# Performance work log

Hardware: AMD Instinct MI355X
Metric: run time of the kernel (lower is better)

## Reference

```python
import jax, jax.numpy as jnp
import numpy as np


def setup_inputs() -> dict:
    key = jax.random.key(0)
    ks = jax.random.split(key, 5)
    B, T, I, H = 64, 2048, 512, 512
    s_in = 1.0 / np.sqrt(I)
    s_h = 1.0 / np.sqrt(H)
    return {
        "x": jax.random.normal(ks[0], (B, T, I), dtype=jnp.float32),
        "Wx": jax.random.normal(ks[1], (4 * H, I), dtype=jnp.float32) * s_in,
        "bx": jax.random.normal(ks[2], (4 * H,), dtype=jnp.float32) * s_in,
        "Wh": jax.random.normal(ks[3], (4 * H, H), dtype=jnp.float32) * s_h,
        "bh": jax.random.normal(ks[4], (4 * H,), dtype=jnp.float32) * s_h,
    }


def reference(x, Wx, bx, Wh, bh):
    B, T, I = x.shape
    H = Wh.shape[1]
    # Precompute input projections for all timesteps (same math, batched GEMM).
    # gates_x: (T, B, 4H)
    gates_x = jnp.einsum('bti,gi->tbg', x, Wx) + bx + bh

    def step(carry, gx):
        h, c = carry
        gates = gx + h @ Wh.T  # (B, 4H)
        i, f, g, o = jnp.split(gates, 4, axis=1)
        i = jax.nn.sigmoid(i)
        f = jax.nn.sigmoid(f)
        g = jnp.tanh(g)
        o = jax.nn.sigmoid(o)
        c = f * c + i * g
        h = o * jnp.tanh(c)
        return (h, c), h

    h0 = jnp.zeros((B, H), dtype=x.dtype)
    c0 = jnp.zeros((B, H), dtype=x.dtype)
    (h_n, c_n), out = jax.lax.scan(step, (h0, c0), gates_x)
    output = jnp.transpose(out, (1, 0, 2))  # (B, T, H)
    return output, (h_n, c_n)
```

## Files before the change

kernel.cpp:

```cpp
#include <hip/hip_runtime.h>
#include <stdint.h>

typedef unsigned short u16;
typedef unsigned int   u32;
typedef unsigned long long u64;

#define B_  64
#define T_  2048
#define I_  512
#define H_  512
#define G_  2048

typedef __attribute__((ext_vector_type(8))) __bf16 bf16x8;
typedef __attribute__((ext_vector_type(4))) float  f32x4;

#define OFF_XB    0ull
#define OFF_GX    134217728ull
#define OFF_WXP   (OFF_GX + 536870912ull)
#define OFF_WHP   (OFF_WXP + 2097152ull)
#define OFF_BIAS  (OFF_WHP + 2097152ull)
#define OFF_HBUF  (OFF_BIAS + 8192ull)
#define WS_NEEDED (OFF_HBUF + 262144ull)

__device__ __forceinline__ float bf2f(u16 u) {
  union { float f; u32 u; } c; c.u = ((u32)u) << 16; return c.f;
}
__device__ __forceinline__ u16 f2bf(float f) {
  union { float f; u32 u; } c; c.f = f;
  u32 u = c.u;
  return (u16)((u + 0x7FFFu + ((u >> 16) & 1u)) >> 16);
}
__device__ __forceinline__ float sigmoidf_(float x) {
  return __fdividef(1.f, 1.f + __expf(-x));
}
__device__ __forceinline__ float tanhf_(float x) {
  return 1.f - __fdividef(2.f, 1.f + __expf(2.f * x));
}
__device__ __forceinline__ void async16(const u16* g, u16* l) {
  __builtin_amdgcn_global_load_lds((const __attribute__((address_space(1))) void*)g,
                                   (__attribute__((address_space(3))) void*)l,
                                   16, 0, 0);
}

__global__ void __launch_bounds__(256)
prep_misc(const float* __restrict__ wx, const float* __restrict__ bx,
          const float* __restrict__ wh, const float* __restrict__ bh,
          u16* __restrict__ wxp, u16* __restrict__ whp,
          float* __restrict__ bias, u32* __restrict__ hbuf0)
{
  int idx = blockIdx.x * 256 + threadIdx.x;
  int n = idx >> 9, k = idx & 511;
  long r = (long)(((n & 3) << 9) | (n >> 2)) * 512 + k;
  wxp[idx] = f2bf(wx[r]);
  whp[idx] = f2bf(wh[r]);
  if (idx < G_) {
    int rb = ((idx & 3) << 9) | (idx >> 2);
    bias[idx] = bx[rb] + bh[rb];
  }
  if (idx < 65536) hbuf0[idx] = 0u;
}

__global__ void __launch_bounds__(256)
conv_x(const float* __restrict__ x, u16* __restrict__ xb)
{
  long idx = ((long)blockIdx.x * 256 + threadIdx.x) * 4;
  float4 v = *(const float4*)(x + idx);
  u64 pk = (u64)f2bf(v.x) | ((u64)f2bf(v.y) << 16) |
           ((u64)f2bf(v.z) << 32) | ((u64)f2bf(v.w) << 48);
  *(u64*)(xb + idx) = pk;
}

__global__ void __launch_bounds__(256)
gemm_gates(const u16* __restrict__ xb, const u16* __restrict__ wxp,
           const float* __restrict__ bias, u16* __restrict__ gx)
{
  __shared__ __align__(16) u16 smem[16384];
  const int tid  = threadIdx.x;
  const int lane = tid & 63;
  const int w    = tid >> 6;
  const int tn   = blockIdx.x;
  const int tm   = blockIdx.y;
  const int wr   = w >> 1, wc = w & 1;

  const u16* gsrc[8];
  u16* ldst[8];
#pragma unroll
  for (int q = 0; q < 8; ++q) {
    int c   = w * 8 + q;
    int isB = c >= 16;
    int cc  = c & 15;
    int rloc = (cc >> 1) * 16 + (lane & 15);
    int koff = (cc & 1) * 32 + ((lane >> 4) << 3);
    if (!isB) {
      int m = tm * 128 + rloc;
      int bb = m & 63, tt = m >> 6;
      gsrc[q] = xb + (long)bb * (T_ * I_) + (long)tt * I_ + koff;
    } else {
      int n = tn * 128 + rloc;
      gsrc[q] = wxp + (long)n * I_ + koff;
    }
    ldst[q] = smem + isB * 8192 + cc * 512;
  }

  f32x4 acc[4][4] = {};
  for (int k0 = 0; k0 < I_; k0 += 64) {
#pragma unroll
    for (int q = 0; q < 8; ++q) async16(gsrc[q] + k0, ldst[q]);
    __syncthreads();
#pragma unroll
    for (int kb = 0; kb < 2; ++kb) {
      bf16x8 a[4], b[4];
#pragma unroll
      for (int i = 0; i < 4; ++i)
        a[i] = *(const bf16x8*)(smem + ((wr * 4 + i) * 2 + kb) * 512 + lane * 8);
#pragma unroll
      for (int j = 0; j < 4; ++j)
        b[j] = *(const bf16x8*)(smem + 8192 + ((wc * 4 + j) * 2 + kb) * 512 + lane * 8);
#pragma unroll
      for (int i = 0; i < 4; ++i)
#pragma unroll
        for (int j = 0; j < 4; ++j)
          acc[i][j] = __builtin_amdgcn_mfma_f32_16x16x32_bf16(a[i], b[j], acc[i][j], 0, 0, 0);
    }
    __syncthreads();
  }

#pragma unroll
  for (int j = 0; j < 4; ++j) {
    int n = tn * 128 + (wc * 4 + j) * 16 + (lane & 15);
    float bv = bias[n];
#pragma unroll
    for (int i = 0; i < 4; ++i) {
      int mbase = tm * 128 + (wr * 4 + i) * 16 + ((lane >> 4) << 2);
#pragma unroll
      for (int r = 0; r < 4; ++r) {
        int m = mbase + r;
        int tt = m >> 6, bb = m & 63;
        gx[(long)tt * (B_ * G_) + (long)bb * G_ + n] = f2bf(acc[i][j][r] + bv);
      }
    }
  }
}

__global__ void __launch_bounds__(256)
lstm_rec(const u16* __restrict__ gx, const u16* __restrict__ whp,
         u64* hbuf, float* __restrict__ out)
{
  __shared__ __align__(16) char lds[32768 + 8192];
  u16*  Hs  = (u16*)lds;
  float* scr = (float*)(lds + 32768);

  const int tid  = threadIdx.x;
  const int lane = tid & 63;
  const int w    = tid >> 6;
  const int bg   = blockIdx.x >> 4;
  const int kg   = blockIdx.x & 15;

  bf16x8 wf0[16], wf1[16];
  {
    const int n0   = kg * 128 + (2 * w) * 16 + (lane & 15);
    const int koff = (lane >> 4) << 3;
#pragma unroll
    for (int kb = 0; kb < 16; ++kb) {
      wf0[kb] = *(const bf16x8*)(whp + (long)n0 * 512 + kb * 32 + koff);
      wf1[kb] = *(const bf16x8*)(whp + (long)(n0 + 16) * 512 + kb * 32 + koff);
    }
  }

  const int srow = tid >> 4;
  const u64* hsrc = hbuf + (long)(bg * 16 + srow) * 256 + (tid & 15);
  const int sl = srow + (((tid & 15) >> 2) << 4);
  u16* sdst = Hs + sl * 8 + 2 * (tid & 3);

  const int id    = lane * 2;
  const int b16   = id >> 3;
  const int klw   = id & 7;
  const int kl    = w * 8 + klw;
  const int kgl   = kg * 32 + kl;
  const int bglob = bg * 16 + b16;

  const u16* gxp0 = gx + (long)bglob * G_ + (long)kgl * 4;
  uint4 gq = *(const uint4*)gxp0;

  u64* hdst = hbuf + (long)bglob * 256 + (kgl >> 1);
  float c0 = 0.f, c1 = 0.f;

  for (int t = 0; t < T_; ++t) {
    const int par = t & 1;

    const u64* hp_ = hsrc + (size_t)par * 16384;
    u64 v[16];
    for (;;) {
      bool ok = true;
#pragma unroll
      for (int s = 0; s < 16; ++s)
        v[s] = __hip_atomic_load(hp_ + s * 16, __ATOMIC_RELAXED, __HIP_MEMORY_SCOPE_AGENT);
#pragma unroll
      for (int s = 0; s < 16; ++s) ok &= ((u32)v[s] == (u32)t);
      if (ok) break;
      __builtin_amdgcn_s_sleep(1);
    }

    u16* sd = sdst + par * 8192;
#pragma unroll
    for (int s = 0; s < 16; ++s)
      *(u32*)(sd + s * 512) = (u32)(v[s] >> 32);
    __syncthreads();

    const u16* Hb = Hs + par * 8192;
    f32x4 acc0a = {0.f,0.f,0.f,0.f}, acc0b = {0.f,0.f,0.f,0.f};
    f32x4 acc1a = {0.f,0.f,0.f,0.f}, acc1b = {0.f,0.f,0.f,0.f};
#pragma unroll
    for (int kb = 0; kb < 16; kb += 2) {
      bf16x8 aA = *(const bf16x8*)(Hb + kb * 512 + lane * 8);
      bf16x8 aB = *(const bf16x8*)(Hb + (kb + 1) * 512 + lane * 8);
      acc0a = __builtin_amdgcn_mfma_f32_16x16x32_bf16(aA, wf0[kb],     acc0a, 0, 0, 0);
      acc1a = __builtin_amdgcn_mfma_f32_16x16x32_bf16(aA, wf1[kb],     acc1a, 0, 0, 0);
      acc0b = __builtin_amdgcn_mfma_f32_16x16x32_bf16(aB, wf0[kb + 1], acc0b, 0, 0, 0);
      acc1b = __builtin_amdgcn_mfma_f32_16x16x32_bf16(aB, wf1[kb + 1], acc1b, 0, 0, 0);
    }
    f32x4 acc0 = acc0a + acc0b;
    f32x4 acc1 = acc1a + acc1b;

    float* sw = scr + w * 512;
    {
      const int colq = (lane & 15) >> 2;
      const int gidx = lane & 3;
      const int bq   = (lane >> 4) << 2;
#pragma unroll
      for (int r = 0; r < 4; ++r) {
        sw[((bq + r) * 8 + colq) * 4 + gidx]     = acc0[r];
        sw[((bq + r) * 8 + 4 + colq) * 4 + gidx] = acc1[r];
      }
    }

    uint4 gqc = gq;
    if (t + 1 < T_) gq = *(const uint4*)(gxp0 + (long)(t + 1) * (B_ * G_));

    const u16* gu = (const u16*)&gqc;
    f32x4 ga = *(const f32x4*)(sw + (b16 * 8 + klw) * 4);
    f32x4 gb = *(const f32x4*)(sw + (b16 * 8 + klw + 1) * 4);

    float i0 = sigmoidf_(ga[0] + bf2f(gu[0]));
    float f0 = sigmoidf_(ga[1] + bf2f(gu[1]));
    float g0 = tanhf_   (ga[2] + bf2f(gu[2]));
    float o0 = sigmoidf_(ga[3] + bf2f(gu[3]));
    float i1 = sigmoidf_(gb[0] + bf2f(gu[4]));
    float f1 = sigmoidf_(gb[1] + bf2f(gu[5]));
    float g1 = tanhf_   (gb[2] + bf2f(gu[6]));
    float o1 = sigmoidf_(gb[3] + bf2f(gu[7]));
    float cn0 = f0 * c0 + i0 * g0;
    float cn1 = f1 * c1 + i1 * g1;
    float h0 = o0 * tanhf_(cn0);
    float h1 = o1 * tanhf_(cn1);
    c0 = cn0;
    c1 = cn1;

    u32 hp = ((u32)f2bf(h1) << 16) | (u32)f2bf(h0);
    u64 tv = ((u64)hp << 32) | (u32)(t + 1);
    __hip_atomic_store(hdst + (size_t)((t + 1) & 1) * 16384, tv,
                       __ATOMIC_RELAXED, __HIP_MEMORY_SCOPE_AGENT);

    float2 hv; hv.x = h0; hv.y = h1;
    *(float2*)(out + ((long)bglob * T_ + t) * H_ + kgl) = hv;

    if (t == T_ - 1) {
      float2 cv; cv.x = cn0; cv.y = cn1;
      *(float2*)(out + (size_t)B_ * T_ * H_ + (long)bglob * H_ + kgl) = hv;
      *(float2*)(out + (size_t)B_ * T_ * H_ + B_ * H_ + (long)bglob * H_ + kgl) = cv;
    }
  }
}

extern "C" void kernel_launch(void* const* d_in, const int* in_sizes, int n_in,
                              void* d_out, int out_size, void* d_ws, size_t ws_size,
                              hipStream_t stream)
{
  (void)in_sizes; (void)n_in; (void)out_size;
  if (ws_size < WS_NEEDED) return;

  const float* x  = (const float*)d_in[0];
  const float* Wx = (const float*)d_in[1];
  const float* bx = (const float*)d_in[2];
  const float* Wh = (const float*)d_in[3];
  const float* bh = (const float*)d_in[4];
  float* out = (float*)d_out;
  char* ws = (char*)d_ws;
  u16* xb     = (u16*)(ws + OFF_XB);
  u16* gx     = (u16*)(ws + OFF_GX);
  u16* wxp    = (u16*)(ws + OFF_WXP);
  u16* whp    = (u16*)(ws + OFF_WHP);
  float* bias = (float*)(ws + OFF_BIAS);
  u64* hbuf   = (u64*)(ws + OFF_HBUF);

  prep_misc<<<4096, 256, 0, stream>>>(Wx, bx, Wh, bh, wxp, whp, bias, (u32*)hbuf);
  conv_x<<<65536, 256, 0, stream>>>(x, xb);
  gemm_gates<<<dim3(16, 1024), 256, 0, stream>>>(xb, wxp, bias, gx);
  lstm_rec<<<64, 256, 0, stream>>>(gx, whp, hbuf, out);
}
```

Before: 5.729 ms.

## Skip own-slice global polling and prefetch next-step hidden-state flags early

```diff
diff --git a/kernel.cpp b/kernel.cpp
--- a/kernel.cpp
+++ b/kernel.cpp
@@ -142,11 +142,11 @@
   }
 }
 
-__global__ void __launch_bounds__(256)
+__global__ void __launch_bounds__(256, 1)
 lstm_rec(const u16* __restrict__ gx, const u16* __restrict__ whp,
          u64* hbuf, float* __restrict__ out)
 {
-  __shared__ __align__(16) char lds[32768 + 8192];
+  __shared__ __align__(16) char lds[32768 + 10240];
   u16*  Hs  = (u16*)lds;
   float* scr = (float*)(lds + 32768);
 
@@ -168,9 +168,10 @@
   }
 
   const int srow = tid >> 4;
-  const u64* hsrc = hbuf + (long)(bg * 16 + srow) * 256 + (tid & 15);
-  const int sl = srow + (((tid & 15) >> 2) << 4);
-  u16* sdst = Hs + sl * 8 + 2 * (tid & 3);
+  const int scol = tid & 15;
+  const u64* hsrc = hbuf + (long)(bg * 16 + srow) * 256 + scol;
+  const int sl = srow + ((scol >> 2) << 4);
+  u16* sdst = Hs + sl * 8 + 2 * (scol & 3);
 
   const int id    = lane * 2;
   const int b16   = id >> 3;
@@ -183,29 +184,46 @@
   uint4 gq = *(const uint4*)gxp0;
 
   u64* hdst = hbuf + (long)bglob * 256 + (kgl >> 1);
+  u16* ownw = Hs + kg * 512 + (b16 + (w << 4)) * 8 + klw;
   float c0 = 0.f, c1 = 0.f;
+
+  *(u32*)ownw = 0u;
+  u64 v[16];
+  v[0] = 0;
+#pragma unroll
+  for (int s = 0; s < 16; ++s)
+    if (s != kg)
+      v[s] = __hip_atomic_load(hsrc + s * 16, __ATOMIC_RELAXED, __HIP_MEMORY_SCOPE_AGENT);
 
   for (int t = 0; t < T_; ++t) {
     const int par = t & 1;
-
     const u64* hp_ = hsrc + (size_t)par * 16384;
-    u64 v[16];
-    for (;;) {
-      bool ok = true;
+
+    bool ok = true;
+#pragma unroll
+    for (int s = 0; s < 16; ++s)
+      if (s != kg) ok &= ((u32)v[s] == (u32)t);
+    while (!ok) {
+      __builtin_amdgcn_s_sleep(1);
 #pragma unroll
       for (int s = 0; s < 16; ++s)
-        v[s] = __hip_atomic_load(hp_ + s * 16, __ATOMIC_RELAXED, __HIP_MEMORY_SCOPE_AGENT);
-#pragma unroll
-      for (int s = 0; s < 16; ++s) ok &= ((u32)v[s] == (u32)t);
-      if (ok) break;
-      __builtin_amdgcn_s_sleep(1);
+        if (s != kg)
+          v[s] = __hip_atomic_load(hp_ + s * 16, __ATOMIC_RELAXED, __HIP_MEMORY_SCOPE_AGENT);
+      ok = true;
+#pragma unroll
+      for (int s = 0; s < 16; ++s)
+        if (s != kg) ok &= ((u32)v[s] == (u32)t);
     }
 
     u16* sd = sdst + par * 8192;
 #pragma unroll
     for (int s = 0; s < 16; ++s)
-      *(u32*)(sd + s * 512) = (u32)(v[s] >> 32);
+      if (s != kg)
+        *(u32*)(sd + s * 512) = (u32)(v[s] >> 32);
     __syncthreads();
+
+    uint4 gcur = gq;
+    if (t + 1 < T_) gq = *(const uint4*)(gxp0 + (long)(t + 1) * (B_ * G_));
 
     const u16* Hb = Hs + par * 8192;
     f32x4 acc0a = {0.f,0.f,0.f,0.f}, acc0b = {0.f,0.f,0.f,0.f};
@@ -222,24 +240,21 @@
     f32x4 acc0 = acc0a + acc0b;
     f32x4 acc1 = acc1a + acc1b;
 
-    float* sw = scr + w * 512;
+    float* sw = scr + w * 640;
     {
       const int colq = (lane & 15) >> 2;
       const int gidx = lane & 3;
       const int bq   = (lane >> 4) << 2;
 #pragma unroll
       for (int r = 0; r < 4; ++r) {
-        sw[((bq + r) * 8 + colq) * 4 + gidx]     = acc0[r];
-        sw[((bq + r) * 8 + 4 + colq) * 4 + gidx] = acc1[r];
+        sw[(bq + r) * 36 + colq * 4 + gidx]       = acc0[r];
+        sw[(bq + r) * 36 + (colq + 4) * 4 + gidx] = acc1[r];
       }
     }
 
-    uint4 gqc = gq;
-    if (t + 1 < T_) gq = *(const uint4*)(gxp0 + (long)(t + 1) * (B_ * G_));
-
-    const u16* gu = (const u16*)&gqc;
-    f32x4 ga = *(const f32x4*)(sw + (b16 * 8 + klw) * 4);
-    f32x4 gb = *(const f32x4*)(sw + (b16 * 8 + klw + 1) * 4);
+    const u16* gu = (const u16*)&gcur;
+    f32x4 ga = *(const f32x4*)(sw + b16 * 36 + klw * 4);
+    f32x4 gb = *(const f32x4*)(sw + b16 * 36 + (klw + 1) * 4);
 
     float i0 = sigmoidf_(ga[0] + bf2f(gu[0]));
     float f0 = sigmoidf_(ga[1] + bf2f(gu[1]));
@@ -256,10 +271,19 @@
     c0 = cn0;
     c1 = cn1;
 
+    if (t + 1 < T_) {
+      const u64* hn_ = hsrc + (size_t)((t + 1) & 1) * 16384;
+#pragma unroll
+      for (int s = 0; s < 16; ++s)
+        if (s != kg)
+          v[s] = __hip_atomic_load(hn_ + s * 16, __ATOMIC_RELAXED, __HIP_MEMORY_SCOPE_AGENT);
+    }
+
     u32 hp = ((u32)f2bf(h1) << 16) | (u32)f2bf(h0);
     u64 tv = ((u64)hp << 32) | (u32)(t + 1);
     __hip_atomic_store(hdst + (size_t)((t + 1) & 1) * 16384, tv,
                        __ATOMIC_RELAXED, __HIP_MEMORY_SCOPE_AGENT);
+    *(u32*)(ownw + ((t + 1) & 1) * 8192) = hp;
 
     float2 hv; hv.x = h0; hv.y = h1;
     *(float2*)(out + ((long)bglob * T_ + t) * H_ + kgl) = hv;
```

Result: slower. 7.863 ms (+37.3%).

## Stage recurrent weights in swizzled LDS and skip polling own h slice

Applied to the files above, without the earlier changes.

```diff
diff --git a/kernel.cpp b/kernel.cpp
--- a/kernel.cpp
+++ b/kernel.cpp
@@ -146,9 +146,10 @@
 lstm_rec(const u16* __restrict__ gx, const u16* __restrict__ whp,
          u64* hbuf, float* __restrict__ out)
 {
-  __shared__ __align__(16) char lds[32768 + 8192];
+  __shared__ __align__(16) char lds[16384 + 131072 + 10240];
   u16*  Hs  = (u16*)lds;
-  float* scr = (float*)(lds + 32768);
+  u16*  LWh = (u16*)(lds + 16384);
+  float* scr = (float*)(lds + 16384 + 131072);
 
   const int tid  = threadIdx.x;
   const int lane = tid & 63;
@@ -156,21 +157,28 @@
   const int bg   = blockIdx.x >> 4;
   const int kg   = blockIdx.x & 15;
 
-  bf16x8 wf0[16], wf1[16];
-  {
-    const int n0   = kg * 128 + (2 * w) * 16 + (lane & 15);
-    const int koff = (lane >> 4) << 3;
-#pragma unroll
-    for (int kb = 0; kb < 16; ++kb) {
-      wf0[kb] = *(const bf16x8*)(whp + (long)n0 * 512 + kb * 32 + koff);
-      wf1[kb] = *(const bf16x8*)(whp + (long)(n0 + 16) * 512 + kb * 32 + koff);
-    }
-  }
+  for (int c = tid; c < 8192; c += 256) {
+    int col = c >> 6;
+    int off = (c & 63) << 4;
+    bf16x8 vw = *(const bf16x8*)(whp + ((long)(kg * 128 + col) << 9) + (off >> 1));
+    *(bf16x8*)((char*)LWh + ((long)col << 10) + (off ^ ((col & 7) << 4))) = vw;
+  }
+
+  const int bcol0 = (w << 5) + (lane & 15);
+  const int bkoff = (lane >> 4) << 4;
+  const int wswz  = (bcol0 & 7) << 4;
+  const int bsw   = bkoff ^ (wswz & 0x30);
+  const char* wbase = (const char*)LWh + (bcol0 << 10);
+  const char* wb0e = wbase + bsw + (wswz & 0x40);
+  const char* wb0o = wbase + bsw - (wswz & 0x40);
+  const char* wb1e = wb0e + (16 << 10);
+  const char* wb1o = wb0o + (16 << 10);
 
   const int srow = tid >> 4;
-  const u64* hsrc = hbuf + (long)(bg * 16 + srow) * 256 + (tid & 15);
-  const int sl = srow + (((tid & 15) >> 2) << 4);
-  u16* sdst = Hs + sl * 8 + 2 * (tid & 3);
+  const int scol = tid & 15;
+  const u64* hsrc = hbuf + (long)(bg * 16 + srow) * 256 + scol;
+  const int sl = srow + ((scol >> 2) << 4);
+  u16* sdst = Hs + sl * 8 + 2 * (scol & 3);
 
   const int id    = lane * 2;
   const int b16   = id >> 3;
@@ -183,54 +191,64 @@
   uint4 gq = *(const uint4*)gxp0;
 
   u64* hdst = hbuf + (long)bglob * 256 + (kgl >> 1);
+  u16* ownw = Hs + kg * 512 + (b16 + (w << 4)) * 8 + klw;
   float c0 = 0.f, c1 = 0.f;
+
+  *(u32*)ownw = 0u;
 
   for (int t = 0; t < T_; ++t) {
     const int par = t & 1;
-
     const u64* hp_ = hsrc + (size_t)par * 16384;
+
     u64 v[16];
+    v[kg] = 0;
     for (;;) {
       bool ok = true;
 #pragma unroll
       for (int s = 0; s < 16; ++s)
-        v[s] = __hip_atomic_load(hp_ + s * 16, __ATOMIC_RELAXED, __HIP_MEMORY_SCOPE_AGENT);
-#pragma unroll
-      for (int s = 0; s < 16; ++s) ok &= ((u32)v[s] == (u32)t);
+        if (s != kg)
+          v[s] = __hip_atomic_load(hp_ + s * 16, __ATOMIC_RELAXED, __HIP_MEMORY_SCOPE_AGENT);
+#pragma unroll
+      for (int s = 0; s < 16; ++s)
+        if (s != kg) ok &= ((u32)v[s] == (u32)t);
       if (ok) break;
       __builtin_amdgcn_s_sleep(1);
     }
 
-    u16* sd = sdst + par * 8192;
 #pragma unroll
     for (int s = 0; s < 16; ++s)
-      *(u32*)(sd + s * 512) = (u32)(v[s] >> 32);
+      if (s != kg)
+        *(u32*)(sdst + s * 512) = (u32)(v[s] >> 32);
     __syncthreads();
 
-    const u16* Hb = Hs + par * 8192;
     f32x4 acc0a = {0.f,0.f,0.f,0.f}, acc0b = {0.f,0.f,0.f,0.f};
     f32x4 acc1a = {0.f,0.f,0.f,0.f}, acc1b = {0.f,0.f,0.f,0.f};
 #pragma unroll
     for (int kb = 0; kb < 16; kb += 2) {
-      bf16x8 aA = *(const bf16x8*)(Hb + kb * 512 + lane * 8);
-      bf16x8 aB = *(const bf16x8*)(Hb + (kb + 1) * 512 + lane * 8);
-      acc0a = __builtin_amdgcn_mfma_f32_16x16x32_bf16(aA, wf0[kb],     acc0a, 0, 0, 0);
-      acc1a = __builtin_amdgcn_mfma_f32_16x16x32_bf16(aA, wf1[kb],     acc1a, 0, 0, 0);
-      acc0b = __builtin_amdgcn_mfma_f32_16x16x32_bf16(aB, wf0[kb + 1], acc0b, 0, 0, 0);
-      acc1b = __builtin_amdgcn_mfma_f32_16x16x32_bf16(aB, wf1[kb + 1], acc1b, 0, 0, 0);
-    }
+      bf16x8 aA  = *(const bf16x8*)(Hs + kb * 512 + lane * 8);
+      bf16x8 aB  = *(const bf16x8*)(Hs + (kb + 1) * 512 + lane * 8);
+      bf16x8 b0A = *(const bf16x8*)(wb0e + kb * 64);
+      bf16x8 b1A = *(const bf16x8*)(wb1e + kb * 64);
+      bf16x8 b0B = *(const bf16x8*)(wb0o + (kb + 1) * 64);
+      bf16x8 b1B = *(const bf16x8*)(wb1o + (kb + 1) * 64);
+      acc0a = __builtin_amdgcn_mfma_f32_16x16x32_bf16(aA, b0A, acc0a, 0, 0, 0);
+      acc1a = __builtin_amdgcn_mfma_f32_16x16x32_bf16(aA, b1A, acc1a, 0, 0, 0);
+      acc0b = __builtin_amdgcn_mfma_f32_16x16x32_bf16(aB, b0B, acc0b, 0, 0, 0);
+      acc1b = __builtin_amdgcn_mfma_f32_16x16x32_bf16(aB, b1B, acc1b, 0, 0, 0);
+    }
+    __syncthreads();
     f32x4 acc0 = acc0a + acc0b;
     f32x4 acc1 = acc1a + acc1b;
 
-    float* sw = scr + w * 512;
+    float* sw = scr + w * 640;
     {
       const int colq = (lane & 15) >> 2;
       const int gidx = lane & 3;
       const int bq   = (lane >> 4) << 2;
 #pragma unroll
       for (int r = 0; r < 4; ++r) {
-        sw[((bq + r) * 8 + colq) * 4 + gidx]     = acc0[r];
-        sw[((bq + r) * 8 + 4 + colq) * 4 + gidx] = acc1[r];
+        sw[(bq + r) * 36 + colq * 4 + gidx]       = acc0[r];
+        sw[(bq + r) * 36 + (colq + 4) * 4 + gidx] = acc1[r];
       }
     }
 
@@ -238,8 +256,8 @@
     if (t + 1 < T_) gq = *(const uint4*)(gxp0 + (long)(t + 1) * (B_ * G_));
 
     const u16* gu = (const u16*)&gqc;
-    f32x4 ga = *(const f32x4*)(sw + (b16 * 8 + klw) * 4);
-    f32x4 gb = *(const f32x4*)(sw + (b16 * 8 + klw + 1) * 4);
+    f32x4 ga = *(const f32x4*)(sw + b16 * 36 + klw * 4);
+    f32x4 gb = *(const f32x4*)(sw + b16 * 36 + (klw + 1) * 4);
 
     float i0 = sigmoidf_(ga[0] + bf2f(gu[0]));
     float f0 = sigmoidf_(ga[1] + bf2f(gu[1]));
@@ -257,6 +275,7 @@
     c1 = cn1;
 
     u32 hp = ((u32)f2bf(h1) << 16) | (u32)f2bf(h0);
+    *(u32*)ownw = hp;
     u64 tv = ((u64)hp << 32) | (u32)(t + 1);
     __hip_atomic_store(hdst + (size_t)((t + 1) & 1) * 16384, tv,
                        __ATOMIC_RELAXED, __HIP_MEMORY_SCOPE_AGENT);
```

New measurement: 7.801 ms. 1.36x slower.

## Split recurrent LSTM block across 8 waves, one gate column tile each

Applied to the files above, without the earlier changes.

```diff
diff --git a/kernel.cpp b/kernel.cpp
--- a/kernel.cpp
+++ b/kernel.cpp
@@ -142,11 +142,11 @@
   }
 }
 
-__global__ void __launch_bounds__(256)
+__global__ void __launch_bounds__(512, 2)
 lstm_rec(const u16* __restrict__ gx, const u16* __restrict__ whp,
          u64* hbuf, float* __restrict__ out)
 {
-  __shared__ __align__(16) char lds[32768 + 8192];
+  __shared__ __align__(16) char lds[32768 + 18432];
   u16*  Hs  = (u16*)lds;
   float* scr = (float*)(lds + 32768);
 
@@ -156,118 +156,102 @@
   const int bg   = blockIdx.x >> 4;
   const int kg   = blockIdx.x & 15;
 
-  bf16x8 wf0[16], wf1[16];
+  bf16x8 wfr[16];
   {
-    const int n0   = kg * 128 + (2 * w) * 16 + (lane & 15);
+    const int n0   = kg * 128 + w * 16 + (lane & 15);
     const int koff = (lane >> 4) << 3;
 #pragma unroll
-    for (int kb = 0; kb < 16; ++kb) {
-      wf0[kb] = *(const bf16x8*)(whp + (long)n0 * 512 + kb * 32 + koff);
-      wf1[kb] = *(const bf16x8*)(whp + (long)(n0 + 16) * 512 + kb * 32 + koff);
-    }
-  }
-
-  const int srow = tid >> 4;
-  const u64* hsrc = hbuf + (long)(bg * 16 + srow) * 256 + (tid & 15);
-  const int sl = srow + (((tid & 15) >> 2) << 4);
-  u16* sdst = Hs + sl * 8 + 2 * (tid & 3);
-
-  const int id    = lane * 2;
-  const int b16   = id >> 3;
-  const int klw   = id & 7;
-  const int kl    = w * 8 + klw;
-  const int kgl   = kg * 32 + kl;
-  const int bglob = bg * 16 + b16;
+    for (int kb = 0; kb < 16; ++kb)
+      wfr[kb] = *(const bf16x8*)(whp + ((long)n0 << 9) + kb * 32 + koff);
+  }
+
+  const int srow  = tid & 15;
+  const int scol2 = tid >> 4;
+  const u64* hsrc = hbuf + (long)(bg * 16 + srow) * 256 + scol2;
+  u16* sdst = Hs + (scol2 >> 4) * 512 +
+              (srow + (((scol2 & 15) >> 2) << 4)) * 8 + 2 * (scol2 & 3);
+
+  const int b16c   = lane >> 2;
+  const int klocal = lane & 3;
+  const int kgl    = kg * 32 + w * 4 + klocal;
+  const int bglob  = bg * 16 + b16c;
 
   const u16* gxp0 = gx + (long)bglob * G_ + (long)kgl * 4;
-  uint4 gq = *(const uint4*)gxp0;
+  u64 gq = *(const u64*)gxp0;
 
   u64* hdst = hbuf + (long)bglob * 256 + (kgl >> 1);
-  float c0 = 0.f, c1 = 0.f;
+  float c0 = 0.f;
 
   for (int t = 0; t < T_; ++t) {
     const int par = t & 1;
-
     const u64* hp_ = hsrc + (size_t)par * 16384;
-    u64 v[16];
+
+    u64 v[8];
     for (;;) {
       bool ok = true;
 #pragma unroll
-      for (int s = 0; s < 16; ++s)
-        v[s] = __hip_atomic_load(hp_ + s * 16, __ATOMIC_RELAXED, __HIP_MEMORY_SCOPE_AGENT);
-#pragma unroll
-      for (int s = 0; s < 16; ++s) ok &= ((u32)v[s] == (u32)t);
+      for (int s = 0; s < 8; ++s)
+        v[s] = __hip_atomic_load(hp_ + s * 32, __ATOMIC_RELAXED, __HIP_MEMORY_SCOPE_AGENT);
+#pragma unroll
+      for (int s = 0; s < 8; ++s) ok &= ((u32)v[s] == (u32)t);
       if (ok) break;
       __builtin_amdgcn_s_sleep(1);
     }
 
     u16* sd = sdst + par * 8192;
 #pragma unroll
-    for (int s = 0; s < 16; ++s)
-      *(u32*)(sd + s * 512) = (u32)(v[s] >> 32);
+    for (int s = 0; s < 8; ++s)
+      *(u32*)(sd + s * 1024) = (u32)(v[s] >> 32);
     __syncthreads();
 
     const u16* Hb = Hs + par * 8192;
-    f32x4 acc0a = {0.f,0.f,0.f,0.f}, acc0b = {0.f,0.f,0.f,0.f};
-    f32x4 acc1a = {0.f,0.f,0.f,0.f}, acc1b = {0.f,0.f,0.f,0.f};
+    f32x4 accP = {0.f,0.f,0.f,0.f}, accQ = {0.f,0.f,0.f,0.f};
 #pragma unroll
     for (int kb = 0; kb < 16; kb += 2) {
       bf16x8 aA = *(const bf16x8*)(Hb + kb * 512 + lane * 8);
       bf16x8 aB = *(const bf16x8*)(Hb + (kb + 1) * 512 + lane * 8);
-      acc0a = __builtin_amdgcn_mfma_f32_16x16x32_bf16(aA, wf0[kb],     acc0a, 0, 0, 0);
-      acc1a = __builtin_amdgcn_mfma_f32_16x16x32_bf16(aA, wf1[kb],     acc1a, 0, 0, 0);
-      acc0b = __builtin_amdgcn_mfma_f32_16x16x32_bf16(aB, wf0[kb + 1], acc0b, 0, 0, 0);
-      acc1b = __builtin_amdgcn_mfma_f32_16x16x32_bf16(aB, wf1[kb + 1], acc1b, 0, 0, 0);
-    }
-    f32x4 acc0 = acc0a + acc0b;
-    f32x4 acc1 = acc1a + acc1b;
-
-    float* sw = scr + w * 512;
+      accP = __builtin_amdgcn_mfma_f32_16x16x32_bf16(aA, wfr[kb],     accP, 0, 0, 0);
+      accQ = __builtin_amdgcn_mfma_f32_16x16x32_bf16(aB, wfr[kb + 1], accQ, 0, 0, 0);
+    }
+    f32x4 acc = accP + accQ;
+
+    float* sw = scr + w * 576;
     {
-      const int colq = (lane & 15) >> 2;
-      const int gidx = lane & 3;
-      const int bq   = (lane >> 4) << 2;
-#pragma unroll
-      for (int r = 0; r < 4; ++r) {
-        sw[((bq + r) * 8 + colq) * 4 + gidx]     = acc0[r];
-        sw[((bq + r) * 8 + 4 + colq) * 4 + gidx] = acc1[r];
-      }
-    }
-
-    uint4 gqc = gq;
-    if (t + 1 < T_) gq = *(const uint4*)(gxp0 + (long)(t + 1) * (B_ * G_));
+      const int c  = lane & 15;
+      const int bq = (lane >> 4) << 2;
+#pragma unroll
+      for (int r = 0; r < 4; ++r)
+        sw[(bq + r) * 36 + c] = acc[r];
+    }
+
+    u64 gqc = gq;
+    if (t + 1 < T_) gq = *(const u64*)(gxp0 + (long)(t + 1) * (B_ * G_));
 
     const u16* gu = (const u16*)&gqc;
-    f32x4 ga = *(const f32x4*)(sw + (b16 * 8 + klw) * 4);
-    f32x4 gb = *(const f32x4*)(sw + (b16 * 8 + klw + 1) * 4);
+    f32x4 ga = *(const f32x4*)(sw + b16c * 36 + klocal * 4);
 
     float i0 = sigmoidf_(ga[0] + bf2f(gu[0]));
     float f0 = sigmoidf_(ga[1] + bf2f(gu[1]));
     float g0 = tanhf_   (ga[2] + bf2f(gu[2]));
     float o0 = sigmoidf_(ga[3] + bf2f(gu[3]));
-    float i1 = sigmoidf_(gb[0] + bf2f(gu[4]));
-    float f1 = sigmoidf_(gb[1] + bf2f(gu[5]));
-    float g1 = tanhf_   (gb[2] + bf2f(gu[6]));
-    float o1 = sigmoidf_(gb[3] + bf2f(gu[7]));
-    float cn0 = f0 * c0 + i0 * g0;
-    float cn1 = f1 * c1 + i1 * g1;
-    float h0 = o0 * tanhf_(cn0);
-    float h1 = o1 * tanhf_(cn1);
-    c0 = cn0;
-    c1 = cn1;
-
-    u32 hp = ((u32)f2bf(h1) << 16) | (u32)f2bf(h0);
-    u64 tv = ((u64)hp << 32) | (u32)(t + 1);
-    __hip_atomic_store(hdst + (size_t)((t + 1) & 1) * 16384, tv,
-                       __ATOMIC_RELAXED, __HIP_MEMORY_SCOPE_AGENT);
-
-    float2 hv; hv.x = h0; hv.y = h1;
-    *(float2*)(out + ((long)bglob * T_ + t) * H_ + kgl) = hv;
-
-    if (t == T_ - 1) {
-      float2 cv; cv.x = cn0; cv.y = cn1;
-      *(float2*)(out + (size_t)B_ * T_ * H_ + (long)bglob * H_ + kgl) = hv;
-      *(float2*)(out + (size_t)B_ * T_ * H_ + B_ * H_ + (long)bglob * H_ + kgl) = cv;
+    float cn = f0 * c0 + i0 * g0;
+    float h  = o0 * tanhf_(cn);
+    c0 = cn;
+
+    float hpart = __shfl_xor(h, 1);
+    float cpart = __shfl_xor(cn, 1);
+    if (!(lane & 1)) {
+      u32 hp = ((u32)f2bf(hpart) << 16) | (u32)f2bf(h);
+      u64 tv = ((u64)hp << 32) | (u32)(t + 1);
+      __hip_atomic_store(hdst + (size_t)((t + 1) & 1) * 16384, tv,
+                         __ATOMIC_RELAXED, __HIP_MEMORY_SCOPE_AGENT);
+      float2 hv; hv.x = h; hv.y = hpart;
+      *(float2*)(out + ((long)bglob * T_ + t) * H_ + kgl) = hv;
+      if (t == T_ - 1) {
+        float2 cv; cv.x = cn; cv.y = cpart;
+        *(float2*)(out + (size_t)B_ * T_ * H_ + (long)bglob * H_ + kgl) = hv;
+        *(float2*)(out + (size_t)B_ * T_ * H_ + B_ * H_ + (long)bglob * H_ + kgl) = cv;
+      }
     }
   }
 }
@@ -296,5 +280,5 @@
   prep_misc<<<4096, 256, 0, stream>>>(Wx, bx, Wh, bh, wxp, whp, bias, (u32*)hbuf);
   conv_x<<<65536, 256, 0, stream>>>(x, xb);
   gemm_gates<<<dim3(16, 1024), 256, 0, stream>>>(xb, wxp, bias, gx);
-  lstm_rec<<<64, 256, 0, stream>>>(gx, whp, hbuf, out);
-}
+  lstm_rec<<<64, 512, 0, stream>>>(gx, whp, hbuf, out);
+}
```

Result: slower. 8.421 ms (+47.0%).
